# Optimization experiments

Hardware: AMD Instinct MI355X
Metric: run time of the kernel (lower is better)

## Reference

```python
import jax, jax.numpy as jnp
from jax import lax
import numpy as np

B, L, D, KSIZE = 8, 2048, 256, 8


def setup_inputs() -> dict:
    key = jax.random.key(0)
    kx, kw, kwin, kb, ktau = jax.random.split(key, 5)
    scale = 1.0 / np.sqrt(D).astype(np.float32)
    x = jax.random.normal(kx, (B, L, D), dtype=jnp.float32)
    weight = jax.random.normal(kw, (D, D), dtype=jnp.float32) * scale
    input_weight = jax.random.normal(kwin, (D, D), dtype=jnp.float32) * scale
    bias = jax.random.normal(kb, (1, D), dtype=jnp.float32)
    # tau = |randn| in the original; offset by 1 to keep 1/tau numerically sane
    tau = jnp.abs(jax.random.normal(ktau, (1, D), dtype=jnp.float32)) + 1.0
    return {"x": x, "weight": weight, "input_weight": input_weight,
            "bias": bias, "tau": tau, "ksize": KSIZE}


def reference(x, weight, input_weight, bias, tau, ksize):
    b, l, d = x.shape
    # get_K: left-pad with (ksize-1) zeros, gather overlapping windows
    xp = jnp.pad(x, ((0, 0), (ksize - 1, 0), (0, 0)))
    idx = jnp.arange(l)[:, None] + jnp.arange(ksize)[None, :]  # (l, ksize)
    windows = xp[:, idx, :]                                    # (b, l, ksize, d)
    xw = windows.reshape(b * l, ksize, d)                      # flatten per-window batch

    inv_tau = 1.0 / tau                                        # (1, d)
    h0 = jnp.zeros((b * l, d), dtype=x.dtype)

    def step(h, xt):
        # SimpleCTRNN update: h += (1/tau) * (-h + relu(h W + x W_in + b))
        h_new = h + inv_tau * (-h + jax.nn.relu(h @ weight + xt @ input_weight + bias))
        return h_new, None

    xs = jnp.swapaxes(xw, 0, 1)                                # (ksize, b*l, d)
    h_last, _ = lax.scan(step, h0, xs)
    # forward() keeps only the last window timestep
    return h_last.reshape(b, l, d)
```

## Files before the change

kernel.cpp:

```cpp
#include <hip/hip_runtime.h>

typedef __bf16 bf16_t;
typedef __bf16 bf16x8 __attribute__((ext_vector_type(8)));
typedef float  f32x4  __attribute__((ext_vector_type(4)));

#define Ldim 2048
#define Ddim 256

__global__ void swz_kernel(const float* __restrict__ w,
                           const float* __restrict__ win,
                           bf16_t* __restrict__ wsw,
                           bf16_t* __restrict__ winsw) {
    int mat = blockIdx.x >> 3, kt = blockIdx.x & 7;
    const float* src = mat ? win : w;
    bf16_t*      dst = mat ? winsw : wsw;
    int ln = threadIdx.x & 63, g = threadIdx.x >> 6;
    int c = ln & 15, q = ln >> 4;
#pragma unroll
    for (int i = 0; i < 4; ++i) {
        int nt = g + 4 * i;
        bf16x8 v;
#pragma unroll
        for (int j = 0; j < 8; ++j)
            v[j] = (bf16_t)src[(kt * 32 + q * 8 + j) * Ddim + nt * 16 + c];
        *(bf16x8*)&dst[((kt * 16 + nt) * 64 + ln) * 8] = v;
    }
}

#define AU_STRIDE 258
#define AU_ROWS   40
#define AU_BYTES  (AU_ROWS * AU_STRIDE * 4)
#define HBUF_BYTES 32768
#define LDS_TOTAL (HBUF_BYTES + AU_BYTES)

extern __shared__ char ldsmem[];

__global__ __launch_bounds__(256, 2)
void rnn_kernel(const float* __restrict__ x,
                const float* __restrict__ bias,
                const float* __restrict__ tau,
                const bf16x8* __restrict__ wsw,
                const bf16x8* __restrict__ winsw,
                float* __restrict__ out)
{
    char*  hb  = ldsmem;
    float* auf = (float*)(ldsmem + HBUF_BYTES);

    const int tid = threadIdx.x;
    const int w   = tid >> 6;
    const int ln  = tid & 63;
    const int c   = ln & 15;
    const int q   = ln >> 4;
    const int tile = blockIdx.x;
    const int bb  = tile >> 6;
    const int l0  = (tile & 63) * 32;

    int   ncol[4];
    float itau[4];
#pragma unroll
    for (int nl = 0; nl < 4; ++nl) {
        ncol[nl] = (w * 4 + nl) * 16 + c;
        itau[nl] = 1.0f / tau[ncol[nl]];
    }

    f32x4 au[3][4];
#pragma unroll
    for (int nl = 0; nl < 4; ++nl) {
        float bv = bias[ncol[nl]];
#pragma unroll
        for (int mt = 0; mt < 3; ++mt) {
            f32x4 t = {bv, bv, bv, bv};
            au[mt][nl] = t;
        }
    }

    const float* xb = x + (long)bb * (Ldim * Ddim);
    const f32x4 zf = {0.f, 0.f, 0.f, 0.f};

    auto loadX = [&](f32x4 (&buf)[3][2], int kt) {
#pragma unroll
        for (int mt = 0; mt < 3; ++mt) {
            int  lrow = l0 - 7 + mt * 16 + c;
            bool ok   = (lrow >= 0) && (lrow < Ldim);
            const f32x4* p = (const f32x4*)(xb + (long)lrow * Ddim + kt * 32 + q * 8);
            buf[mt][0] = ok ? p[0] : zf;
            buf[mt][1] = ok ? p[1] : zf;
        }
    };
    auto loadW = [&](bf16x8 (&wb)[4], int kt) {
#pragma unroll
        for (int nl = 0; nl < 4; ++nl)
            wb[nl] = winsw[(kt * 16 + 4 * w + nl) * 64 + ln];
    };
    auto step1 = [&](const f32x4 (&buf)[3][2], const bf16x8 (&wb)[4]) {
        bf16x8 aF[3];
#pragma unroll
        for (int mt = 0; mt < 3; ++mt)
#pragma unroll
            for (int jj = 0; jj < 4; ++jj) {
                aF[mt][jj]     = (bf16_t)buf[mt][0][jj];
                aF[mt][jj + 4] = (bf16_t)buf[mt][1][jj];
            }
#pragma unroll
        for (int nl = 0; nl < 4; ++nl)
#pragma unroll
            for (int mt = 0; mt < 3; ++mt)
                au[mt][nl] = __builtin_amdgcn_mfma_f32_16x16x32_bf16(
                    aF[mt], wb[nl], au[mt][nl], 0, 0, 0);
    };

    {
        f32x4  x0[3][2], x1[3][2];
        bf16x8 w0[4], w1[4];
        loadX(x0, 0); loadW(w0, 0);
#pragma unroll 1
        for (int kk = 0; kk < 4; ++kk) {
            loadX(x1, 2 * kk + 1); loadW(w1, 2 * kk + 1);
            step1(x0, w0);
            if (kk < 3) { loadX(x0, 2 * kk + 2); loadW(w0, 2 * kk + 2); }
            step1(x1, w1);
        }
    }

#pragma unroll
    for (int mt = 0; mt < 3; ++mt)
#pragma unroll
        for (int nl = 0; nl < 4; ++nl)
#pragma unroll
            for (int r = 0; r < 4; ++r) {
                int row = mt * 16 + q * 4 + r;
                if (row < 39)
                    auf[row * AU_STRIDE + ncol[nl]] = au[mt][nl][r];
            }

    f32x4 h[2][4];
#pragma unroll
    for (int mt = 0; mt < 2; ++mt)
#pragma unroll
        for (int nl = 0; nl < 4; ++nl)
#pragma unroll
            for (int r = 0; r < 4; ++r)
                h[mt][nl][r] = itau[nl] * fmaxf(au[mt][nl][r], 0.0f);

    bf16x8 bfr[8][4];
#pragma unroll
    for (int kt = 0; kt < 8; ++kt)
#pragma unroll
        for (int nl = 0; nl < 4; ++nl)
            bfr[kt][nl] = wsw[(kt * 16 + 4 * w + nl) * 64 + ln];

    int offn[4];
#pragma unroll
    for (int nl = 0; nl < 4; ++nl) {
        int kk = ncol[nl];
        offn[nl] = (kk >> 5) * 1024 + ((kk >> 3) & 3) * 64 + q * 16 + (kk & 7) * 2;
    }
    const int permln = (((ln & 3) << 4) | ((ln >> 4) << 2) | ((ln >> 2) & 3)) * 16;

#pragma unroll
    for (int mt = 0; mt < 2; ++mt)
#pragma unroll
        for (int nl = 0; nl < 4; ++nl)
#pragma unroll
            for (int r = 0; r < 4; ++r)
                *(bf16_t*)(hb + mt * 8192 + r * 256 + offn[nl]) =
                    (bf16_t)h[mt][nl][r];
    __syncthreads();

    int cur = 0;
#pragma unroll 1
    for (int t = 1; t < 8; ++t) {
        char* pc = hb + cur * 16384;
        char* pn = hb + (cur ^ 1) * 16384;
        const float* urow = auf + (q * 4 + t) * AU_STRIDE;
#pragma unroll
        for (int mt = 0; mt < 2; ++mt) {
            f32x4 acc[4];
#pragma unroll
            for (int nl = 0; nl < 4; ++nl) {
                f32x4 a;
#pragma unroll
                for (int r = 0; r < 4; ++r)
                    a[r] = urow[(mt * 16 + r) * AU_STRIDE + ncol[nl]];
                acc[nl] = a;
            }
            __builtin_amdgcn_s_setprio(1);
#pragma unroll
            for (int kt = 0; kt < 8; ++kt) {
                bf16x8 aF = *(const bf16x8*)(pc + (mt * 8 + kt) * 1024 + permln);
#pragma unroll
                for (int nl = 0; nl < 4; ++nl)
                    acc[nl] = __builtin_amdgcn_mfma_f32_16x16x32_bf16(
                        aF, bfr[kt][nl], acc[nl], 0, 0, 0);
            }
            __builtin_amdgcn_s_setprio(0);
#pragma unroll
            for (int nl = 0; nl < 4; ++nl)
#pragma unroll
                for (int r = 0; r < 4; ++r) {
                    float hh = h[mt][nl][r];
                    float s  = fmaxf(acc[nl][r], 0.0f);
                    h[mt][nl][r] = hh + itau[nl] * (s - hh);
                }
            if (t < 7) {
#pragma unroll
                for (int nl = 0; nl < 4; ++nl)
#pragma unroll
                    for (int r = 0; r < 4; ++r)
                        *(bf16_t*)(pn + mt * 8192 + r * 256 + offn[nl]) =
                            (bf16_t)h[mt][nl][r];
            }
        }
        if (t < 7) __syncthreads();
        cur ^= 1;
    }

    float* ob = out + ((long)bb * Ldim + l0) * Ddim;
#pragma unroll
    for (int mt = 0; mt < 2; ++mt)
#pragma unroll
        for (int nl = 0; nl < 4; ++nl)
#pragma unroll
            for (int r = 0; r < 4; ++r)
                ob[(mt * 16 + 4 * q + r) * Ddim + ncol[nl]] = h[mt][nl][r];
}

extern "C" void kernel_launch(void* const* d_in, const int* in_sizes, int n_in,
                              void* d_out, int out_size, void* d_ws, size_t ws_size,
                              hipStream_t stream) {
    const float* x            = (const float*)d_in[0];
    const float* weight       = (const float*)d_in[1];
    const float* input_weight = (const float*)d_in[2];
    const float* bias         = (const float*)d_in[3];
    const float* tau          = (const float*)d_in[4];
    (void)in_sizes; (void)n_in; (void)out_size; (void)ws_size;

    bf16_t* wsw   = (bf16_t*)d_ws;
    bf16_t* winsw = wsw + 65536;

    static bool attr_set = false;
    if (!attr_set) {
        (void)hipFuncSetAttribute((const void*)rnn_kernel,
                                  hipFuncAttributeMaxDynamicSharedMemorySize,
                                  LDS_TOTAL);
        attr_set = true;
    }

    swz_kernel<<<16, 256, 0, stream>>>(weight, input_weight, wsw, winsw);
    rnn_kernel<<<512, 256, LDS_TOTAL, stream>>>(x, bias, tau,
                                                (const bf16x8*)wsw,
                                                (const bf16x8*)winsw,
                                                (float*)d_out);
}
```

Baseline: 107.4 us.

## Split input projection into separate GEMM kernel writing transposed U to workspace

The input projection x·W_in + bias moves out of the recurrent kernel into its own GEMM kernel that writes U transposed to global workspace. The old version recomputed 39 rows per 32-row tile because of the window halo, and the new one computes each row once. Bias-padded leading rows handle the left pad. The recurrent kernel now reads U from global memory with one step of register prefetch instead of staging it in LDS, which cuts LDS use, but it adds a kernel launch and a global round trip for U.

```diff
diff --git a/kernel.cpp b/kernel.cpp
--- a/kernel.cpp
+++ b/kernel.cpp
@@ -7,11 +7,18 @@
 #define Ldim 2048
 #define Ddim 256
 
+#define USTRIDE 2064
+#define UOFF    8
+#define U_WS_BYTE_OFF (1 << 20)
+
 __global__ void swz_kernel(const float* __restrict__ w,
                            const float* __restrict__ win,
+                           const float* __restrict__ bias,
                            bf16_t* __restrict__ wsw,
-                           bf16_t* __restrict__ winsw) {
-    int mat = blockIdx.x >> 3, kt = blockIdx.x & 7;
+                           bf16_t* __restrict__ winsw,
+                           float* __restrict__ Ut) {
+    int blk = blockIdx.x;
+    int mat = blk >> 3, kt = blk & 7;
     const float* src = mat ? win : w;
     bf16_t*      dst = mat ? winsw : wsw;
     int ln = threadIdx.x & 63, g = threadIdx.x >> 6;
@@ -25,27 +32,20 @@
             v[j] = (bf16_t)src[(kt * 32 + q * 8 + j) * Ddim + nt * 16 + c];
         *(bf16x8*)&dst[((kt * 16 + nt) * 64 + ln) * 8] = v;
     }
-}
-
-#define AU_STRIDE 258
-#define AU_ROWS   40
-#define AU_BYTES  (AU_ROWS * AU_STRIDE * 4)
-#define HBUF_BYTES 32768
-#define LDS_TOTAL (HBUF_BYTES + AU_BYTES)
-
-extern __shared__ char ldsmem[];
+    if (blk < 8) {
+        float bv = bias[threadIdx.x];
+        float* p = Ut + ((long)(blk << 8) + threadIdx.x) * USTRIDE;
+#pragma unroll
+        for (int i = 0; i < 8; ++i) p[i] = bv;
+    }
+}
 
 __global__ __launch_bounds__(256, 2)
-void rnn_kernel(const float* __restrict__ x,
-                const float* __restrict__ bias,
-                const float* __restrict__ tau,
-                const bf16x8* __restrict__ wsw,
-                const bf16x8* __restrict__ winsw,
-                float* __restrict__ out)
+void gemm_u_kernel(const float* __restrict__ x,
+                   const float* __restrict__ bias,
+                   const bf16x8* __restrict__ winsw,
+                   float* __restrict__ Ut)
 {
-    char*  hb  = ldsmem;
-    float* auf = (float*)(ldsmem + HBUF_BYTES);
-
     const int tid = threadIdx.x;
     const int w   = tid >> 6;
     const int ln  = tid & 63;
@@ -55,36 +55,30 @@
     const int bb  = tile >> 6;
     const int l0  = (tile & 63) * 32;
 
-    int   ncol[4];
-    float itau[4];
-#pragma unroll
-    for (int nl = 0; nl < 4; ++nl) {
-        ncol[nl] = (w * 4 + nl) * 16 + c;
-        itau[nl] = 1.0f / tau[ncol[nl]];
-    }
-
-    f32x4 au[3][4];
+    int ncol[4];
+#pragma unroll
+    for (int nl = 0; nl < 4; ++nl) ncol[nl] = (w * 4 + nl) * 16 + c;
+
+    f32x4 au[2][4];
 #pragma unroll
     for (int nl = 0; nl < 4; ++nl) {
         float bv = bias[ncol[nl]];
 #pragma unroll
-        for (int mt = 0; mt < 3; ++mt) {
+        for (int mt = 0; mt < 2; ++mt) {
             f32x4 t = {bv, bv, bv, bv};
             au[mt][nl] = t;
         }
     }
 
     const float* xb = x + (long)bb * (Ldim * Ddim);
-    const f32x4 zf = {0.f, 0.f, 0.f, 0.f};
-
-    auto loadX = [&](f32x4 (&buf)[3][2], int kt) {
-#pragma unroll
-        for (int mt = 0; mt < 3; ++mt) {
-            int  lrow = l0 - 7 + mt * 16 + c;
-            bool ok   = (lrow >= 0) && (lrow < Ldim);
-            const f32x4* p = (const f32x4*)(xb + (long)lrow * Ddim + kt * 32 + q * 8);
-            buf[mt][0] = ok ? p[0] : zf;
-            buf[mt][1] = ok ? p[1] : zf;
+
+    auto loadX = [&](f32x4 (&buf)[2][2], int kt) {
+#pragma unroll
+        for (int mt = 0; mt < 2; ++mt) {
+            const f32x4* p = (const f32x4*)(xb + (long)(l0 + mt * 16 + c) * Ddim
+                                            + kt * 32 + q * 8);
+            buf[mt][0] = p[0];
+            buf[mt][1] = p[1];
         }
     };
     auto loadW = [&](bf16x8 (&wb)[4], int kt) {
@@ -92,10 +86,10 @@
         for (int nl = 0; nl < 4; ++nl)
             wb[nl] = winsw[(kt * 16 + 4 * w + nl) * 64 + ln];
     };
-    auto step1 = [&](const f32x4 (&buf)[3][2], const bf16x8 (&wb)[4]) {
-        bf16x8 aF[3];
-#pragma unroll
-        for (int mt = 0; mt < 3; ++mt)
+    auto step1 = [&](const f32x4 (&buf)[2][2], const bf16x8 (&wb)[4]) {
+        bf16x8 aF[2];
+#pragma unroll
+        for (int mt = 0; mt < 2; ++mt)
 #pragma unroll
             for (int jj = 0; jj < 4; ++jj) {
                 aF[mt][jj]     = (bf16_t)buf[mt][0][jj];
@@ -104,13 +98,13 @@
 #pragma unroll
         for (int nl = 0; nl < 4; ++nl)
 #pragma unroll
-            for (int mt = 0; mt < 3; ++mt)
+            for (int mt = 0; mt < 2; ++mt)
                 au[mt][nl] = __builtin_amdgcn_mfma_f32_16x16x32_bf16(
                     aF[mt], wb[nl], au[mt][nl], 0, 0, 0);
     };
 
     {
-        f32x4  x0[3][2], x1[3][2];
+        f32x4  x0[2][2], x1[2][2];
         bf16x8 w0[4], w1[4];
         loadX(x0, 0); loadW(w0, 0);
 #pragma unroll 1
@@ -123,31 +117,57 @@
     }
 
 #pragma unroll
-    for (int mt = 0; mt < 3; ++mt)
+    for (int mt = 0; mt < 2; ++mt)
+#pragma unroll
+        for (int nl = 0; nl < 4; ++nl)
+            *(f32x4*)&Ut[((long)((bb << 8) + ncol[nl])) * USTRIDE
+                         + UOFF + l0 + mt * 16 + 4 * q] = au[mt][nl];
+}
+
+__global__ __launch_bounds__(256, 2)
+void rnn_kernel(const float* __restrict__ tau,
+                const bf16x8* __restrict__ wsw,
+                const float* __restrict__ Ut,
+                float* __restrict__ out)
+{
+    __shared__ char hb[32768];
+
+    const int tid = threadIdx.x;
+    const int w   = tid >> 6;
+    const int ln  = tid & 63;
+    const int c   = ln & 15;
+    const int q   = ln >> 4;
+    const int tile = blockIdx.x;
+    const int bb  = tile >> 6;
+    const int l0  = (tile & 63) * 32;
+
+    int   ncol[4];
+    float itau[4];
+    long  ubase[4];
+#pragma unroll
+    for (int nl = 0; nl < 4; ++nl) {
+        ncol[nl]  = (w * 4 + nl) * 16 + c;
+        itau[nl]  = 1.0f / tau[ncol[nl]];
+        ubase[nl] = ((long)((bb << 8) + ncol[nl])) * USTRIDE + UOFF + l0;
+    }
+
+    bf16x8 bfr[8][4];
+#pragma unroll
+    for (int kt = 0; kt < 8; ++kt)
+#pragma unroll
+        for (int nl = 0; nl < 4; ++nl)
+            bfr[kt][nl] = wsw[(kt * 16 + 4 * w + nl) * 64 + ln];
+
+    f32x4 h[2][4];
+#pragma unroll
+    for (int mt = 0; mt < 2; ++mt)
 #pragma unroll
         for (int nl = 0; nl < 4; ++nl)
 #pragma unroll
             for (int r = 0; r < 4; ++r) {
-                int row = mt * 16 + q * 4 + r;
-                if (row < 39)
-                    auf[row * AU_STRIDE + ncol[nl]] = au[mt][nl][r];
-            }
-
-    f32x4 h[2][4];
-#pragma unroll
-    for (int mt = 0; mt < 2; ++mt)
-#pragma unroll
-        for (int nl = 0; nl < 4; ++nl)
-#pragma unroll
-            for (int r = 0; r < 4; ++r)
-                h[mt][nl][r] = itau[nl] * fmaxf(au[mt][nl][r], 0.0f);
-
-    bf16x8 bfr[8][4];
-#pragma unroll
-    for (int kt = 0; kt < 8; ++kt)
-#pragma unroll
-        for (int nl = 0; nl < 4; ++nl)
-            bfr[kt][nl] = wsw[(kt * 16 + 4 * w + nl) * 64 + ln];
+                float u = Ut[ubase[nl] - 7 + mt * 16 + 4 * q + r];
+                h[mt][nl][r] = itau[nl] * fmaxf(u, 0.0f);
+            }
 
     int offn[4];
 #pragma unroll
@@ -165,6 +185,16 @@
             for (int r = 0; r < 4; ++r)
                 *(bf16_t*)(hb + mt * 8192 + r * 256 + offn[nl]) =
                     (bf16_t)h[mt][nl][r];
+
+    float up[2][4][4];
+#pragma unroll
+    for (int mt = 0; mt < 2; ++mt)
+#pragma unroll
+        for (int nl = 0; nl < 4; ++nl)
+#pragma unroll
+            for (int r = 0; r < 4; ++r)
+                up[mt][nl][r] = Ut[ubase[nl] - 7 + 1 + mt * 16 + 4 * q + r];
+
     __syncthreads();
 
     int cur = 0;
@@ -172,17 +202,21 @@
     for (int t = 1; t < 8; ++t) {
         char* pc = hb + cur * 16384;
         char* pn = hb + (cur ^ 1) * 16384;
-        const float* urow = auf + (q * 4 + t) * AU_STRIDE;
 #pragma unroll
         for (int mt = 0; mt < 2; ++mt) {
             f32x4 acc[4];
 #pragma unroll
             for (int nl = 0; nl < 4; ++nl) {
-                f32x4 a;
-#pragma unroll
-                for (int r = 0; r < 4; ++r)
-                    a[r] = urow[(mt * 16 + r) * AU_STRIDE + ncol[nl]];
+                f32x4 a = {up[mt][nl][0], up[mt][nl][1], up[mt][nl][2], up[mt][nl][3]};
                 acc[nl] = a;
+            }
+            if (t < 7) {
+#pragma unroll
+                for (int nl = 0; nl < 4; ++nl)
+#pragma unroll
+                    for (int r = 0; r < 4; ++r)
+                        up[mt][nl][r] =
+                            Ut[ubase[nl] - 7 + (t + 1) + mt * 16 + 4 * q + r];
             }
             __builtin_amdgcn_s_setprio(1);
 #pragma unroll
@@ -237,18 +271,9 @@
 
     bf16_t* wsw   = (bf16_t*)d_ws;
     bf16_t* winsw = wsw + 65536;
-
-    static bool attr_set = false;
-    if (!attr_set) {
-        (void)hipFuncSetAttribute((const void*)rnn_kernel,
-                                  hipFuncAttributeMaxDynamicSharedMemorySize,
-                                  LDS_TOTAL);
-        attr_set = true;
-    }
-
-    swz_kernel<<<16, 256, 0, stream>>>(weight, input_weight, wsw, winsw);
-    rnn_kernel<<<512, 256, LDS_TOTAL, stream>>>(x, bias, tau,
-                                                (const bf16x8*)wsw,
-                                                (const bf16x8*)winsw,
-                                                (float*)d_out);
-}
+    float*  Ut    = (float*)((char*)d_ws + U_WS_BYTE_OFF);
+
+    swz_kernel<<<16, 256, 0, stream>>>(weight, input_weight, bias, wsw, winsw, Ut);
+    gemm_u_kernel<<<512, 256, 0, stream>>>(x, bias, (const bf16x8*)winsw, Ut);
+    rnn_kernel<<<512, 256, 0, stream>>>(tau, (const bf16x8*)wsw, Ut, (float*)d_out);
+}
```

Measured after the change: 122.4 us. 14.0% more time.

## Process two 32-row tiles per block and interleave their recurrence steps

Applied to the files above, without the earlier changes.

Each block now handles 64 sequence positions as two independent 32-row halves (A and B), so the grid drops from 512 to 256 blocks and occupancy from 2 to 1 block per CU. Within each timestep, the A-half epilogue and LDS stores are placed between the B-half MFMA chains, which lets one half's elementwise work overlap the other half's matrix work. It also reduces redundant halo input-projection rows (7 extra per 64 instead of per 32). The cost is more registers and LDS per block, and with 256 blocks on a 256-CU part each CU runs a single 4-wave block, leaving little latency hiding across blocks.

```diff
diff --git a/kernel.cpp b/kernel.cpp
--- a/kernel.cpp
+++ b/kernel.cpp
@@ -28,14 +28,14 @@
 }
 
 #define AU_STRIDE 258
-#define AU_ROWS   40
+#define AU_ROWS   72
 #define AU_BYTES  (AU_ROWS * AU_STRIDE * 4)
-#define HBUF_BYTES 32768
+#define HBUF_BYTES 65536
 #define LDS_TOTAL (HBUF_BYTES + AU_BYTES)
 
 extern __shared__ char ldsmem[];
 
-__global__ __launch_bounds__(256, 2)
+__global__ __launch_bounds__(256, 1)
 void rnn_kernel(const float* __restrict__ x,
                 const float* __restrict__ bias,
                 const float* __restrict__ tau,
@@ -43,7 +43,8 @@
                 const bf16x8* __restrict__ winsw,
                 float* __restrict__ out)
 {
-    char*  hb  = ldsmem;
+    char*  hbA = ldsmem;
+    char*  hbB = ldsmem + 32768;
     float* auf = (float*)(ldsmem + HBUF_BYTES);
 
     const int tid = threadIdx.x;
@@ -51,9 +52,9 @@
     const int ln  = tid & 63;
     const int c   = ln & 15;
     const int q   = ln >> 4;
-    const int tile = blockIdx.x;
-    const int bb  = tile >> 6;
-    const int l0  = (tile & 63) * 32;
+    const int blk = blockIdx.x;
+    const int bb  = blk >> 5;
+    const int l0  = (blk & 31) * 64;
 
     int   ncol[4];
     float itau[4];
@@ -63,12 +64,12 @@
         itau[nl] = 1.0f / tau[ncol[nl]];
     }
 
-    f32x4 au[3][4];
+    f32x4 au[5][4];
 #pragma unroll
     for (int nl = 0; nl < 4; ++nl) {
         float bv = bias[ncol[nl]];
 #pragma unroll
-        for (int mt = 0; mt < 3; ++mt) {
+        for (int mt = 0; mt < 5; ++mt) {
             f32x4 t = {bv, bv, bv, bv};
             au[mt][nl] = t;
         }
@@ -77,9 +78,9 @@
     const float* xb = x + (long)bb * (Ldim * Ddim);
     const f32x4 zf = {0.f, 0.f, 0.f, 0.f};
 
-    auto loadX = [&](f32x4 (&buf)[3][2], int kt) {
-#pragma unroll
-        for (int mt = 0; mt < 3; ++mt) {
+    auto loadX = [&](f32x4 (&buf)[5][2], int kt) {
+#pragma unroll
+        for (int mt = 0; mt < 5; ++mt) {
             int  lrow = l0 - 7 + mt * 16 + c;
             bool ok   = (lrow >= 0) && (lrow < Ldim);
             const f32x4* p = (const f32x4*)(xb + (long)lrow * Ddim + kt * 32 + q * 8);
@@ -92,10 +93,10 @@
         for (int nl = 0; nl < 4; ++nl)
             wb[nl] = winsw[(kt * 16 + 4 * w + nl) * 64 + ln];
     };
-    auto step1 = [&](const f32x4 (&buf)[3][2], const bf16x8 (&wb)[4]) {
-        bf16x8 aF[3];
-#pragma unroll
-        for (int mt = 0; mt < 3; ++mt)
+    auto step1 = [&](const f32x4 (&buf)[5][2], const bf16x8 (&wb)[4]) {
+        bf16x8 aF[5];
+#pragma unroll
+        for (int mt = 0; mt < 5; ++mt)
 #pragma unroll
             for (int jj = 0; jj < 4; ++jj) {
                 aF[mt][jj]     = (bf16_t)buf[mt][0][jj];
@@ -104,13 +105,13 @@
 #pragma unroll
         for (int nl = 0; nl < 4; ++nl)
 #pragma unroll
-            for (int mt = 0; mt < 3; ++mt)
+            for (int mt = 0; mt < 5; ++mt)
                 au[mt][nl] = __builtin_amdgcn_mfma_f32_16x16x32_bf16(
                     aF[mt], wb[nl], au[mt][nl], 0, 0, 0);
     };
 
     {
-        f32x4  x0[3][2], x1[3][2];
+        f32x4  x0[5][2], x1[5][2];
         bf16x8 w0[4], w1[4];
         loadX(x0, 0); loadW(w0, 0);
 #pragma unroll 1
@@ -123,19 +124,19 @@
     }
 
 #pragma unroll
-    for (int mt = 0; mt < 3; ++mt)
+    for (int mt = 0; mt < 5; ++mt)
 #pragma unroll
         for (int nl = 0; nl < 4; ++nl)
 #pragma unroll
             for (int r = 0; r < 4; ++r) {
                 int row = mt * 16 + q * 4 + r;
-                if (row < 39)
+                if (row < AU_ROWS)
                     auf[row * AU_STRIDE + ncol[nl]] = au[mt][nl][r];
             }
 
-    f32x4 h[2][4];
-#pragma unroll
-    for (int mt = 0; mt < 2; ++mt)
+    f32x4 h[4][4];
+#pragma unroll
+    for (int mt = 0; mt < 4; ++mt)
 #pragma unroll
         for (int nl = 0; nl < 4; ++nl)
 #pragma unroll
@@ -162,62 +163,106 @@
 #pragma unroll
         for (int nl = 0; nl < 4; ++nl)
 #pragma unroll
-            for (int r = 0; r < 4; ++r)
-                *(bf16_t*)(hb + mt * 8192 + r * 256 + offn[nl]) =
+            for (int r = 0; r < 4; ++r) {
+                *(bf16_t*)(hbA + mt * 8192 + r * 256 + offn[nl]) =
                     (bf16_t)h[mt][nl][r];
+                *(bf16_t*)(hbB + mt * 8192 + r * 256 + offn[nl]) =
+                    (bf16_t)h[mt + 2][nl][r];
+            }
     __syncthreads();
 
     int cur = 0;
 #pragma unroll 1
     for (int t = 1; t < 8; ++t) {
-        char* pc = hb + cur * 16384;
-        char* pn = hb + (cur ^ 1) * 16384;
-        const float* urow = auf + (q * 4 + t) * AU_STRIDE;
-#pragma unroll
-        for (int mt = 0; mt < 2; ++mt) {
-            f32x4 acc[4];
-#pragma unroll
-            for (int nl = 0; nl < 4; ++nl) {
-                f32x4 a;
+        char* pAc = hbA + cur * 16384;
+        char* pAn = hbA + (cur ^ 1) * 16384;
+        char* pBc = hbB + cur * 16384;
+        char* pBn = hbB + (cur ^ 1) * 16384;
+
+        f32x4 accA[2][4];
+#pragma unroll
+        for (int mt = 0; mt < 2; ++mt)
+#pragma unroll
+            for (int nl = 0; nl < 4; ++nl)
 #pragma unroll
                 for (int r = 0; r < 4; ++r)
-                    a[r] = urow[(mt * 16 + r) * AU_STRIDE + ncol[nl]];
-                acc[nl] = a;
-            }
-            __builtin_amdgcn_s_setprio(1);
-#pragma unroll
-            for (int kt = 0; kt < 8; ++kt) {
-                bf16x8 aF = *(const bf16x8*)(pc + (mt * 8 + kt) * 1024 + permln);
+                    accA[mt][nl][r] =
+                        auf[(mt * 16 + 4 * q + r + t) * AU_STRIDE + ncol[nl]];
+        bf16x8 aFA[2][8];
+#pragma unroll
+        for (int mt = 0; mt < 2; ++mt)
+#pragma unroll
+            for (int kt = 0; kt < 8; ++kt)
+                aFA[mt][kt] = *(const bf16x8*)(pAc + (mt * 8 + kt) * 1024 + permln);
+#pragma unroll
+        for (int mt = 0; mt < 2; ++mt)
+#pragma unroll
+            for (int kt = 0; kt < 8; ++kt)
 #pragma unroll
                 for (int nl = 0; nl < 4; ++nl)
-                    acc[nl] = __builtin_amdgcn_mfma_f32_16x16x32_bf16(
-                        aF, bfr[kt][nl], acc[nl], 0, 0, 0);
-            }
-            __builtin_amdgcn_s_setprio(0);
+                    accA[mt][nl] = __builtin_amdgcn_mfma_f32_16x16x32_bf16(
+                        aFA[mt][kt], bfr[kt][nl], accA[mt][nl], 0, 0, 0);
+
+        f32x4 accB[2][4];
+#pragma unroll
+        for (int mt = 0; mt < 2; ++mt)
+#pragma unroll
+            for (int nl = 0; nl < 4; ++nl)
+#pragma unroll
+                for (int r = 0; r < 4; ++r)
+                    accB[mt][nl][r] =
+                        auf[(32 + mt * 16 + 4 * q + r + t) * AU_STRIDE + ncol[nl]];
+        bf16x8 aFB[2][8];
+#pragma unroll
+        for (int mt = 0; mt < 2; ++mt)
+#pragma unroll
+            for (int kt = 0; kt < 8; ++kt)
+                aFB[mt][kt] = *(const bf16x8*)(pBc + (mt * 8 + kt) * 1024 + permln);
+
+#pragma unroll
+        for (int mt = 0; mt < 2; ++mt)
 #pragma unroll
             for (int nl = 0; nl < 4; ++nl)
 #pragma unroll
                 for (int r = 0; r < 4; ++r) {
                     float hh = h[mt][nl][r];
-                    float s  = fmaxf(acc[nl][r], 0.0f);
-                    h[mt][nl][r] = hh + itau[nl] * (s - hh);
+                    float s  = fmaxf(accA[mt][nl][r], 0.0f);
+                    hh = hh + itau[nl] * (s - hh);
+                    h[mt][nl][r] = hh;
+                    if (t < 7)
+                        *(bf16_t*)(pAn + mt * 8192 + r * 256 + offn[nl]) = (bf16_t)hh;
                 }
-            if (t < 7) {
+
+#pragma unroll
+        for (int mt = 0; mt < 2; ++mt)
+#pragma unroll
+            for (int kt = 0; kt < 8; ++kt)
 #pragma unroll
                 for (int nl = 0; nl < 4; ++nl)
-#pragma unroll
-                    for (int r = 0; r < 4; ++r)
-                        *(bf16_t*)(pn + mt * 8192 + r * 256 + offn[nl]) =
-                            (bf16_t)h[mt][nl][r];
-            }
-        }
+                    accB[mt][nl] = __builtin_amdgcn_mfma_f32_16x16x32_bf16(
+                        aFB[mt][kt], bfr[kt][nl], accB[mt][nl], 0, 0, 0);
+
+#pragma unroll
+        for (int mt = 0; mt < 2; ++mt)
+#pragma unroll
+            for (int nl = 0; nl < 4; ++nl)
+#pragma unroll
+                for (int r = 0; r < 4; ++r) {
+                    float hh = h[mt + 2][nl][r];
+                    float s  = fmaxf(accB[mt][nl][r], 0.0f);
+                    hh = hh + itau[nl] * (s - hh);
+                    h[mt + 2][nl][r] = hh;
+                    if (t < 7)
+                        *(bf16_t*)(pBn + mt * 8192 + r * 256 + offn[nl]) = (bf16_t)hh;
+                }
+
         if (t < 7) __syncthreads();
         cur ^= 1;
     }
 
     float* ob = out + ((long)bb * Ldim + l0) * Ddim;
 #pragma unroll
-    for (int mt = 0; mt < 2; ++mt)
+    for (int mt = 0; mt < 4; ++mt)
 #pragma unroll
         for (int nl = 0; nl < 4; ++nl)
 #pragma unroll
@@ -247,7 +292,7 @@
     }
 
     swz_kernel<<<16, 256, 0, stream>>>(weight, input_weight, wsw, winsw);
-    rnn_kernel<<<512, 256, LDS_TOTAL, stream>>>(x, bias, tau,
+    rnn_kernel<<<256, 256, LDS_TOTAL, stream>>>(x, bias, tau,
                                                 (const bf16x8*)wsw,
                                                 (const bf16x8*)winsw,
                                                 (float*)d_out);
```

After: 115.5 us. +7.5%, slower.
